# Kernel optimization log

Hardware: AMD Instinct MI355X
Metric: run time of the kernel (lower is better)

Reference implementation:

```python
import jax, jax.numpy as jnp
import numpy as np

THRESHOLD = 0.05


def ternary_project(w, threshold=THRESHOLD, use_ste=True):
    # scale: mean |w| over all axes except the last (per-output-column scale)
    reduce_axes = tuple(range(w.ndim - 1))
    scale = jnp.mean(jnp.abs(w), axis=reduce_axes, keepdims=True)
    ternary = jnp.where(jnp.abs(w) < threshold, 0.0, jnp.sign(w)) * scale
    if use_ste:
        return w + jax.lax.stop_gradient(ternary - w)
    return ternary


def setup_inputs() -> dict:
    key = jax.random.key(0)
    kx, kw = jax.random.split(key)
    B, S, D, O = 8, 2048, 4096, 4096
    x = jax.random.normal(kx, (B, S, D), dtype=jnp.float32)
    w = jax.random.normal(kw, (D, O), dtype=jnp.float32) * 0.02  # small init like VarianceScaling
    b = jnp.zeros((O,), dtype=jnp.float32)
    return {"x": x, "w": w, "b": b}


def reference(x, w, b):
    y = x @ ternary_project(w, threshold=THRESHOLD, use_ste=True)
    return y + b
```

## Files before the change

### kernel.cpp

```cpp
#include <hip/hip_runtime.h>
#include <stdint.h>

typedef int i32x4 __attribute__((ext_vector_type(4)));

#define D_DIM 4096
#define O_DIM 4096
#define M_DIM 16384
#define THRESH 0.05f


__device__ __forceinline__ void gld16(const void* g, void* l) {
  __builtin_amdgcn_global_load_lds(
      (const __attribute__((address_space(1))) uint32_t*)(uintptr_t)g,
      (__attribute__((address_space(3))) uint32_t*)(uint32_t)(uintptr_t)l,
      16, 0, 0);
}

__device__ __forceinline__ int tern_i8(float v) {
  return (__builtin_fabsf(v) < THRESH) ? 0 : (v > 0.f ? 1 : -1);
}


__global__ void k_scale_part(const float* __restrict__ w, float* __restrict__ part) {
  const int cg = blockIdx.x & 63;
  const int dz = blockIdx.x >> 6;
  const int tx = threadIdx.x & 63;
  const int ty = threadIdx.x >> 6;
  const int o = cg * 64 + tx;
  float s = 0.f;
  const float* p = w + (size_t)(dz * 512 + ty) * O_DIM + o;
  for (int i = 0; i < 128; ++i) {
    s += __builtin_fabsf(*p);
    p += 4 * O_DIM;
  }
  __shared__ float red[4][64];
  red[ty][tx] = s;
  __syncthreads();
  if (ty == 0) part[dz * O_DIM + o] = (red[0][tx] + red[1][tx]) + (red[2][tx] + red[3][tx]);
}

__global__ void k_scale_fin(const float* __restrict__ part, float* __restrict__ scale) {
  const int o = blockIdx.x * 256 + threadIdx.x;
  float s = 0.f;
#pragma unroll
  for (int z = 0; z < 8; ++z) s += part[z * O_DIM + o];
  scale[o] = s * (1.0f / 4096.0f);
}

__global__ void k_tern_q(const float* __restrict__ w, char* __restrict__ btq) {
  __shared__ char tile[64][68];
  const int ot = blockIdx.x & 63;
  const int dt = blockIdx.x >> 6;
  const int o0 = ot * 64, d0 = dt * 64;
  const int tx = threadIdx.x & 15, ty = threadIdx.x >> 4;
#pragma unroll
  for (int j = 0; j < 4; ++j) {
    const int r = ty + 16 * j;
    const float4 v = *(const float4*)&w[(size_t)(d0 + r) * O_DIM + o0 + tx * 4];
    uint32_t u = (uint32_t)(tern_i8(v.x) & 0xFF) |
                 ((uint32_t)(tern_i8(v.y) & 0xFF) << 8) |
                 ((uint32_t)(tern_i8(v.z) & 0xFF) << 16) |
                 ((uint32_t)(tern_i8(v.w) & 0xFF) << 24);
    *(uint32_t*)&tile[r][tx * 4] = u;
  }
  __syncthreads();
#pragma unroll
  for (int j = 0; j < 4; ++j) {
    const int orow = ty + 16 * j;
    uint32_t u = (uint32_t)((uint8_t)tile[tx * 4 + 0][orow]) |
                 ((uint32_t)((uint8_t)tile[tx * 4 + 1][orow]) << 8) |
                 ((uint32_t)((uint8_t)tile[tx * 4 + 2][orow]) << 16) |
                 ((uint32_t)((uint8_t)tile[tx * 4 + 3][orow]) << 24);
    *(uint32_t*)&btq[(size_t)(o0 + orow) * D_DIM + d0 + tx * 4] = u;
  }
}

__global__ void k_quant(const float* __restrict__ x, char* __restrict__ xq,
                        float* __restrict__ sx) {
  const int row = blockIdx.x;
  const int t = threadIdx.x;
  const float* xr = x + (size_t)row * D_DIM + t * 16;
  float4 v[4];
#pragma unroll
  for (int i = 0; i < 4; ++i) v[i] = *(const float4*)(xr + i * 4);
  float m = 0.f;
#pragma unroll
  for (int i = 0; i < 4; ++i) {
    m = fmaxf(m, fmaxf(fmaxf(__builtin_fabsf(v[i].x), __builtin_fabsf(v[i].y)),
                       fmaxf(__builtin_fabsf(v[i].z), __builtin_fabsf(v[i].w))));
  }
#pragma unroll
  for (int off = 32; off >= 1; off >>= 1) m = fmaxf(m, __shfl_xor(m, off, 64));
  __shared__ float wm[4];
  if ((t & 63) == 0) wm[t >> 6] = m;
  __syncthreads();
  const float rm = fmaxf(fmaxf(wm[0], wm[1]), fmaxf(wm[2], wm[3]));
  const float inv = (rm > 0.f) ? 127.0f / rm : 0.0f;
  int4 o;
  int* op = (int*)&o;
#pragma unroll
  for (int i = 0; i < 4; ++i) {
    const float* f = (const float*)&v[i];
    uint32_t u = 0;
#pragma unroll
    for (int j = 0; j < 4; ++j) {
      float q = __builtin_rintf(f[j] * inv);
      q = fmaxf(-127.f, fminf(127.f, q));
      u |= ((uint32_t)((int)q & 0xFF)) << (8 * j);
    }
    op[i] = (int)u;
  }
  *(int4*)(xq + (size_t)row * D_DIM + t * 16) = o;
  if (t == 0) sx[row] = (rm > 0.f) ? rm * (1.0f / 127.0f) : 0.0f;
}


#define BAR() __builtin_amdgcn_s_barrier()
#define SB0() __builtin_amdgcn_sched_barrier(0)
#define LGKM0()                                         \
  do {                                                  \
    asm volatile("s_waitcnt lgkmcnt(0)" ::: "memory");  \
    __builtin_amdgcn_sched_barrier(0);                  \
  } while (0)
#define VMW(n) asm volatile("s_waitcnt vmcnt(" #n ")" ::: "memory")

#define STAGE_A(d, h, kv)                                                    \
  do {                                                                       \
    gld16(pA##h##_0 + (size_t)(kv) * 128,                                    \
          smem + (d)*32768 + (h)*16384 + t * 16);                            \
    gld16(pA##h##_1 + (size_t)(kv) * 128,                                    \
          smem + (d)*32768 + (h)*16384 + 8192 + t * 16);                     \
  } while (0)
#define STAGE_B(d, h, kv)                                                    \
  do {                                                                       \
    gld16(pB##h##_0 + (size_t)(kv) * 128,                                    \
          smem + 65536 + (d)*32768 + (h)*16384 + t * 16);                    \
    gld16(pB##h##_1 + (size_t)(kv) * 128,                                    \
          smem + 65536 + (d)*32768 + (h)*16384 + 8192 + t * 16);             \
  } while (0)

#define READ_A(d, mh)                                                   \
  do {                                                                  \
    const char* ab_ = smem + (d)*32768 + wr * 16384 + (mh)*8192;        \
    _Pragma("unroll") for (int m4 = 0; m4 < 4; ++m4) {                  \
      aq[mh][0][m4] = *(const i32x4*)(ab_ + m4 * 2048 + aLane);         \
      aq[mh][1][m4] = *(const i32x4*)(ab_ + m4 * 2048 + (aLane ^ 64));  \
    }                                                                   \
  } while (0)

#define READ_B(db, pp)                                                       \
  do {                                                                       \
    const char* bb_ = smem + 65536 + (db)*32768 + hb * 16384 + hw8192;       \
    _Pragma("unroll") for (int nh = 0; nh < 2; ++nh)                         \
    _Pragma("unroll") for (int n2 = 0; n2 < 2; ++n2) {                       \
      bq[pp][nh][0][n2] =                                                    \
          *(const i32x4*)(bb_ + nh * 4096 + n2 * 2048 + aLane);              \
      bq[pp][nh][1][n2] =                                                    \
          *(const i32x4*)(bb_ + nh * 4096 + n2 * 2048 + (aLane ^ 64));       \
    }                                                                        \
  } while (0)

#define MQ(mh, nh, pp)                                                        \
  do {                                                                        \
    __builtin_amdgcn_s_setprio(1);                                            \
    _Pragma("unroll") for (int kk = 0; kk < 2; ++kk)                          \
    _Pragma("unroll") for (int m4 = 0; m4 < 4; ++m4)                          \
    _Pragma("unroll") for (int n2 = 0; n2 < 2; ++n2)                          \
        acc[(mh)*4 + m4][(nh)*2 + n2] =                                       \
            __builtin_amdgcn_mfma_i32_16x16x64_i8(                            \
                aq[mh][kk][m4], bq[pp][nh][kk][n2],                           \
                acc[(mh)*4 + m4][(nh)*2 + n2], 0, 0, 0);                      \
    __builtin_amdgcn_s_setprio(0);                                            \
  } while (0)

#define TILE(d, pp, kv)                                                  \
  do {                                                                   \
    READ_A(d, 0); STAGE_B(d, 0, kv);                                     \
    BAR(); LGKM0(); MQ(0, 0, pp); BAR();                                 \
    READ_A(d, 1); STAGE_B(d, 1, kv);                                     \
    BAR(); LGKM0(); MQ(0, 1, pp); BAR();                                 \
    STAGE_A(d, 0, kv);                                                   \
    BAR(); __builtin_amdgcn_sched_barrier(0); MQ(1, 0, pp); VMW(10);     \
    BAR();                                                               \
    READ_B((d) ^ 1, (pp) ^ 1); STAGE_A(d, 1, kv);                        \
    BAR(); __builtin_amdgcn_sched_barrier(0); MQ(1, 1, pp); VMW(8);      \
    BAR();                                                               \
  } while (0)

__global__ __launch_bounds__(512, 2) void k_gemm8(
    const char* __restrict__ A,
    const char* __restrict__ B,
    const float* __restrict__ sx, const float* __restrict__ scale,
    const float* __restrict__ bias, float* __restrict__ C) {
  __shared__ __align__(16) char smem[131072];

  const int bid = blockIdx.x;
  const int wg = (bid & 7) * 128 + (bid >> 3);
  const int mb = wg >> 4, nb = wg & 15;
  const int mBase = mb * 256, nBase = nb * 256;

  const int t = threadIdx.x;
  const int lane = t & 63, wid = t >> 6;
  const int wr = wid >> 2, wc = wid & 3;
  const int hb = wc >> 1;
  const int hw8192 = (wc & 1) * 8192;
  const int r16 = lane & 15, kq = lane >> 4;
  const int aLane = r16 * 128 + ((kq ^ (lane & 7)) << 4);

  const int q1 = 512 + t;
  const int sr0 = t >> 3, sg0 = (t & 7) ^ (sr0 & 7);
  const int sr1 = q1 >> 3, sg1 = (q1 & 7) ^ (sr1 & 7);

  const char* pA0_0 = A + (size_t)(mBase + sr0) * D_DIM + sg0 * 16;
  const char* pA0_1 = A + (size_t)(mBase + sr1) * D_DIM + sg1 * 16;
  const char* pA1_0 = A + (size_t)(mBase + 128 + sr0) * D_DIM + sg0 * 16;
  const char* pA1_1 = A + (size_t)(mBase + 128 + sr1) * D_DIM + sg1 * 16;
  const char* pB0_0 = B + (size_t)(nBase + sr0) * D_DIM + sg0 * 16;
  const char* pB0_1 = B + (size_t)(nBase + sr1) * D_DIM + sg1 * 16;
  const char* pB1_0 = B + (size_t)(nBase + 128 + sr0) * D_DIM + sg0 * 16;
  const char* pB1_1 = B + (size_t)(nBase + 128 + sr1) * D_DIM + sg1 * 16;

  i32x4 acc[8][4] = {};
  i32x4 aq[2][2][4];
  i32x4 bq[2][2][2][2];

  STAGE_B(0, 0, 0); STAGE_B(0, 1, 0); STAGE_A(0, 0, 0); STAGE_A(0, 1, 0);
  STAGE_B(1, 0, 1); STAGE_B(1, 1, 1); STAGE_A(1, 0, 1); STAGE_A(1, 1, 1);
  VMW(8);
  BAR();
  RB_PROLOGUE:;
  READ_B(0, 0);
  LGKM0();
  BAR();

  for (int T = 0; T < 32; T += 2) {
    TILE(0, 0, (T + 2) & 31);
    TILE(1, 1, (T + 3) & 31);
  }
  VMW(0);

  float sxr[8][4];
#pragma unroll
  for (int mi = 0; mi < 8; ++mi) {
    const int gr0 = mBase + wr * 128 + mi * 16 + kq * 4;
#pragma unroll
    for (int r = 0; r < 4; ++r) sxr[mi][r] = sx[gr0 + r];
  }
#pragma unroll
  for (int ni = 0; ni < 4; ++ni) {
    const int gc = nBase + wc * 64 + ni * 16 + r16;
    const float sw = scale[gc];
    const float bb = bias[gc];
#pragma unroll
    for (int mi = 0; mi < 8; ++mi) {
      const int gr0 = mBase + wr * 128 + mi * 16 + kq * 4;
#pragma unroll
      for (int r = 0; r < 4; ++r) {
        C[(size_t)(gr0 + r) * O_DIM + gc] =
            (float)acc[mi][ni][r] * (sxr[mi][r] * sw) + bb;
      }
    }
  }
}


extern "C" void kernel_launch(void* const* d_in, const int* in_sizes, int n_in,
                              void* d_out, int out_size, void* d_ws, size_t ws_size,
                              hipStream_t stream) {
  const float* x = (const float*)d_in[0];
  const float* w = (const float*)d_in[1];
  const float* bias = (const float*)d_in[2];
  float* out = (float*)d_out;

  const size_t XQ_OFF = 0;
  const size_t BT_OFF = (size_t)M_DIM * D_DIM;
  const size_t SX_OFF = BT_OFF + (size_t)O_DIM * D_DIM;
  const size_t PART_OFF = SX_OFF + (size_t)M_DIM * 4;
  const size_t SCALE_OFF = PART_OFF + 8 * O_DIM * 4;
  const size_t NEED = SCALE_OFF + O_DIM * 4;
  if (ws_size < NEED) return;

  char* ws = (char*)d_ws;
  char* xq = ws + XQ_OFF;
  char* btq = ws + BT_OFF;
  float* sx = (float*)(ws + SX_OFF);
  float* part = (float*)(ws + PART_OFF);
  float* scale = (float*)(ws + SCALE_OFF);

  k_scale_part<<<512, 256, 0, stream>>>(w, part);
  k_scale_fin<<<16, 256, 0, stream>>>(part, scale);
  k_tern_q<<<64 * 64, 256, 0, stream>>>(w, btq);
  k_quant<<<M_DIM, 256, 0, stream>>>(x, xq, sx);
  k_gemm8<<<1024, 512, 0, stream>>>(xq, btq, sx, scale, bias, out);
}
```

Before: 373.5 us.

## Fuse weight scale reduction into ternary quantize and restructure GEMM LDS schedule

The separate k_scale_part pass over w is removed. Per-column |w| partial sums are now computed inside k_tern_q from the already-loaded tile and written to a 64-way partial buffer, which k_scale_fin then reduces. Separately, the GEMM inner tile schedule is reorganized: both A halves are read before the first MFMA group, waits become partial lgkmcnt counts, and fewer barriers are used, so LDS reads overlap more with MFMA work. This trades one fewer read of w for a larger partial buffer and a riskier wait/barrier ordering.

```diff
diff --git a/kernel.cpp b/kernel.cpp
--- a/kernel.cpp
+++ b/kernel.cpp
@@ -21,48 +21,32 @@
 }
 
 
-__global__ void k_scale_part(const float* __restrict__ w, float* __restrict__ part) {
-  const int cg = blockIdx.x & 63;
-  const int dz = blockIdx.x >> 6;
-  const int tx = threadIdx.x & 63;
-  const int ty = threadIdx.x >> 6;
-  const int o = cg * 64 + tx;
-  float s = 0.f;
-  const float* p = w + (size_t)(dz * 512 + ty) * O_DIM + o;
-  for (int i = 0; i < 128; ++i) {
-    s += __builtin_fabsf(*p);
-    p += 4 * O_DIM;
-  }
-  __shared__ float red[4][64];
-  red[ty][tx] = s;
-  __syncthreads();
-  if (ty == 0) part[dz * O_DIM + o] = (red[0][tx] + red[1][tx]) + (red[2][tx] + red[3][tx]);
-}
-
-__global__ void k_scale_fin(const float* __restrict__ part, float* __restrict__ scale) {
-  const int o = blockIdx.x * 256 + threadIdx.x;
-  float s = 0.f;
-#pragma unroll
-  for (int z = 0; z < 8; ++z) s += part[z * O_DIM + o];
-  scale[o] = s * (1.0f / 4096.0f);
-}
-
-__global__ void k_tern_q(const float* __restrict__ w, char* __restrict__ btq) {
+__global__ void k_tern_q(const float* __restrict__ w, char* __restrict__ btq,
+                         float* __restrict__ part) {
   __shared__ char tile[64][68];
+  __shared__ float sred[16][68];
   const int ot = blockIdx.x & 63;
   const int dt = blockIdx.x >> 6;
   const int o0 = ot * 64, d0 = dt * 64;
-  const int tx = threadIdx.x & 15, ty = threadIdx.x >> 4;
+  const int t = threadIdx.x;
+  const int tx = t & 15, ty = t >> 4;
+  float s0 = 0.f, s1 = 0.f, s2 = 0.f, s3 = 0.f;
 #pragma unroll
   for (int j = 0; j < 4; ++j) {
     const int r = ty + 16 * j;
     const float4 v = *(const float4*)&w[(size_t)(d0 + r) * O_DIM + o0 + tx * 4];
+    s0 += __builtin_fabsf(v.x); s1 += __builtin_fabsf(v.y);
+    s2 += __builtin_fabsf(v.z); s3 += __builtin_fabsf(v.w);
     uint32_t u = (uint32_t)(tern_i8(v.x) & 0xFF) |
                  ((uint32_t)(tern_i8(v.y) & 0xFF) << 8) |
                  ((uint32_t)(tern_i8(v.z) & 0xFF) << 16) |
                  ((uint32_t)(tern_i8(v.w) & 0xFF) << 24);
     *(uint32_t*)&tile[r][tx * 4] = u;
   }
+  sred[ty][tx * 4 + 0] = s0;
+  sred[ty][tx * 4 + 1] = s1;
+  sred[ty][tx * 4 + 2] = s2;
+  sred[ty][tx * 4 + 3] = s3;
   __syncthreads();
 #pragma unroll
   for (int j = 0; j < 4; ++j) {
@@ -73,6 +57,20 @@
                  ((uint32_t)((uint8_t)tile[tx * 4 + 3][orow]) << 24);
     *(uint32_t*)&btq[(size_t)(o0 + orow) * D_DIM + d0 + tx * 4] = u;
   }
+  if (t < 64) {
+    float s = 0.f;
+#pragma unroll
+    for (int i = 0; i < 16; ++i) s += sred[i][t];
+    part[(size_t)dt * O_DIM + o0 + t] = s;
+  }
+}
+
+__global__ void k_scale_fin(const float* __restrict__ part, float* __restrict__ scale) {
+  const int o = blockIdx.x * 256 + threadIdx.x;
+  float s = 0.f;
+#pragma unroll
+  for (int z = 0; z < 64; ++z) s += part[(size_t)z * O_DIM + o];
+  scale[o] = s * (1.0f / 4096.0f);
 }
 
 __global__ void k_quant(const float* __restrict__ x, char* __restrict__ xq,
@@ -117,11 +115,7 @@
 
 #define BAR() __builtin_amdgcn_s_barrier()
 #define SB0() __builtin_amdgcn_sched_barrier(0)
-#define LGKM0()                                         \
-  do {                                                  \
-    asm volatile("s_waitcnt lgkmcnt(0)" ::: "memory");  \
-    __builtin_amdgcn_sched_barrier(0);                  \
-  } while (0)
+#define LGKM(n) asm volatile("s_waitcnt lgkmcnt(" #n ")" ::: "memory")
 #define VMW(n) asm volatile("s_waitcnt vmcnt(" #n ")" ::: "memory")
 
 #define STAGE_A(d, h, kv)                                                    \
@@ -175,15 +169,16 @@
 
 #define TILE(d, pp, kv)                                                  \
   do {                                                                   \
-    READ_A(d, 0); STAGE_B(d, 0, kv);                                     \
-    BAR(); LGKM0(); MQ(0, 0, pp); BAR();                                 \
-    READ_A(d, 1); STAGE_B(d, 1, kv);                                     \
-    BAR(); LGKM0(); MQ(0, 1, pp); BAR();                                 \
-    STAGE_A(d, 0, kv);                                                   \
-    BAR(); __builtin_amdgcn_sched_barrier(0); MQ(1, 0, pp); VMW(10);     \
+    READ_A(d, 0); READ_A(d, 1); STAGE_B(d, 0, kv); STAGE_B(d, 1, kv);    \
+    BAR(); LGKM(8); SB0();                                               \
+    MQ(0, 0, pp); MQ(0, 1, pp);                                          \
     BAR();                                                               \
-    READ_B((d) ^ 1, (pp) ^ 1); STAGE_A(d, 1, kv);                        \
-    BAR(); __builtin_amdgcn_sched_barrier(0); MQ(1, 1, pp); VMW(8);      \
+    STAGE_A(d, 0, kv); STAGE_A(d, 1, kv);                                \
+    LGKM(0); SB0();                                                      \
+    MQ(1, 0, pp);                                                        \
+    VMW(8); BAR();                                                       \
+    READ_B((d) ^ 1, (pp) ^ 1); SB0();                                    \
+    MQ(1, 1, pp);                                                        \
     BAR();                                                               \
   } while (0)
 
@@ -228,9 +223,8 @@
   STAGE_B(1, 0, 1); STAGE_B(1, 1, 1); STAGE_A(1, 0, 1); STAGE_A(1, 1, 1);
   VMW(8);
   BAR();
-  RB_PROLOGUE:;
   READ_B(0, 0);
-  LGKM0();
+  LGKM(0); SB0();
   BAR();
 
   for (int T = 0; T < 32; T += 2) {
@@ -276,7 +270,7 @@
   const size_t BT_OFF = (size_t)M_DIM * D_DIM;
   const size_t SX_OFF = BT_OFF + (size_t)O_DIM * D_DIM;
   const size_t PART_OFF = SX_OFF + (size_t)M_DIM * 4;
-  const size_t SCALE_OFF = PART_OFF + 8 * O_DIM * 4;
+  const size_t SCALE_OFF = PART_OFF + (size_t)64 * O_DIM * 4;
   const size_t NEED = SCALE_OFF + O_DIM * 4;
   if (ws_size < NEED) return;
 
@@ -287,9 +281,8 @@
   float* part = (float*)(ws + PART_OFF);
   float* scale = (float*)(ws + SCALE_OFF);
 
-  k_scale_part<<<512, 256, 0, stream>>>(w, part);
+  k_tern_q<<<64 * 64, 256, 0, stream>>>(w, btq, part);
   k_scale_fin<<<16, 256, 0, stream>>>(part, scale);
-  k_tern_q<<<64 * 64, 256, 0, stream>>>(w, btq);
   k_quant<<<M_DIM, 256, 0, stream>>>(x, xq, sx);
   k_gemm8<<<1024, 512, 0, stream>>>(xq, btq, sx, scale, bias, out);
 }
```

Result: slower. 381.4 us (+2.1%).

## Shrink int8 GEMM tile to 128x128 with 256-thread blocks and simpler pipeline

Applied to the files above, without the earlier changes.

Replaces the 256x256 tile, 512-thread GEMM with a 128x128 tile, 4-wave block using 64 KiB LDS. Each wave now computes a 64x64 output sub-tile, and the staging and compute schedule per K step is simplified. The block remap changes so that each XCD handles a contiguous band of N columns. Smaller tiles cut per-block LDS and registers, which may allow more resident blocks, but they halve data reuse and double global and LDS traffic per MFMA.

```diff
diff --git a/kernel.cpp b/kernel.cpp
--- a/kernel.cpp
+++ b/kernel.cpp
@@ -117,132 +117,121 @@
 
 #define BAR() __builtin_amdgcn_s_barrier()
 #define SB0() __builtin_amdgcn_sched_barrier(0)
-#define LGKM0()                                         \
-  do {                                                  \
-    asm volatile("s_waitcnt lgkmcnt(0)" ::: "memory");  \
-    __builtin_amdgcn_sched_barrier(0);                  \
-  } while (0)
+#define LGKM(n) asm volatile("s_waitcnt lgkmcnt(" #n ")" ::: "memory")
 #define VMW(n) asm volatile("s_waitcnt vmcnt(" #n ")" ::: "memory")
 
-#define STAGE_A(d, h, kv)                                                    \
-  do {                                                                       \
-    gld16(pA##h##_0 + (size_t)(kv) * 128,                                    \
-          smem + (d)*32768 + (h)*16384 + t * 16);                            \
-    gld16(pA##h##_1 + (size_t)(kv) * 128,                                    \
-          smem + (d)*32768 + (h)*16384 + 8192 + t * 16);                     \
-  } while (0)
-#define STAGE_B(d, h, kv)                                                    \
-  do {                                                                       \
-    gld16(pB##h##_0 + (size_t)(kv) * 128,                                    \
-          smem + 65536 + (d)*32768 + (h)*16384 + t * 16);                    \
-    gld16(pB##h##_1 + (size_t)(kv) * 128,                                    \
-          smem + 65536 + (d)*32768 + (h)*16384 + 8192 + t * 16);             \
-  } while (0)
-
-#define READ_A(d, mh)                                                   \
-  do {                                                                  \
-    const char* ab_ = smem + (d)*32768 + wr * 16384 + (mh)*8192;        \
-    _Pragma("unroll") for (int m4 = 0; m4 < 4; ++m4) {                  \
-      aq[mh][0][m4] = *(const i32x4*)(ab_ + m4 * 2048 + aLane);         \
-      aq[mh][1][m4] = *(const i32x4*)(ab_ + m4 * 2048 + (aLane ^ 64));  \
-    }                                                                   \
-  } while (0)
-
-#define READ_B(db, pp)                                                       \
-  do {                                                                       \
-    const char* bb_ = smem + 65536 + (db)*32768 + hb * 16384 + hw8192;       \
-    _Pragma("unroll") for (int nh = 0; nh < 2; ++nh)                         \
-    _Pragma("unroll") for (int n2 = 0; n2 < 2; ++n2) {                       \
-      bq[pp][nh][0][n2] =                                                    \
-          *(const i32x4*)(bb_ + nh * 4096 + n2 * 2048 + aLane);              \
-      bq[pp][nh][1][n2] =                                                    \
-          *(const i32x4*)(bb_ + nh * 4096 + n2 * 2048 + (aLane ^ 64));       \
-    }                                                                        \
-  } while (0)
-
-#define MQ(mh, nh, pp)                                                        \
+#define STAGE_A(d, kv)                                              \
+  do {                                                              \
+    gld16(pA0 + (size_t)(kv) * 128, smem + (d)*16384 + t * 16);     \
+    gld16(pA1 + (size_t)(kv) * 128, smem + (d)*16384 + 4096 + t * 16); \
+    gld16(pA2 + (size_t)(kv) * 128, smem + (d)*16384 + 8192 + t * 16); \
+    gld16(pA3 + (size_t)(kv) * 128, smem + (d)*16384 + 12288 + t * 16); \
+  } while (0)
+#define STAGE_B(d, kv)                                              \
+  do {                                                              \
+    gld16(pB0 + (size_t)(kv) * 128, smem + 32768 + (d)*16384 + t * 16); \
+    gld16(pB1 + (size_t)(kv) * 128, smem + 32768 + (d)*16384 + 4096 + t * 16); \
+    gld16(pB2 + (size_t)(kv) * 128, smem + 32768 + (d)*16384 + 8192 + t * 16); \
+    gld16(pB3 + (size_t)(kv) * 128, smem + 32768 + (d)*16384 + 12288 + t * 16); \
+  } while (0)
+
+#define RA(d)                                                          \
+  do {                                                                 \
+    const char* ab_ = smem + (d)*16384 + (wr * 64 + r16) * 128;        \
+    _Pragma("unroll") for (int m4 = 0; m4 < 4; ++m4) {                 \
+      aq[0][m4] = *(const i32x4*)(ab_ + m4 * 2048 + slot0);            \
+      aq[1][m4] = *(const i32x4*)(ab_ + m4 * 2048 + (slot0 ^ 64));     \
+    }                                                                  \
+  } while (0)
+#define RB(db)                                                         \
+  do {                                                                 \
+    const char* bb_ = smem + 32768 + (db)*16384 + (wc * 64 + r16) * 128; \
+    _Pragma("unroll") for (int n4 = 0; n4 < 4; ++n4) {                 \
+      bq[0][n4] = *(const i32x4*)(bb_ + n4 * 2048 + slot0);            \
+      bq[1][n4] = *(const i32x4*)(bb_ + n4 * 2048 + (slot0 ^ 64));     \
+    }                                                                  \
+  } while (0)
+
+#define MQ(kk)                                                                \
   do {                                                                        \
     __builtin_amdgcn_s_setprio(1);                                            \
-    _Pragma("unroll") for (int kk = 0; kk < 2; ++kk)                          \
     _Pragma("unroll") for (int m4 = 0; m4 < 4; ++m4)                          \
-    _Pragma("unroll") for (int n2 = 0; n2 < 2; ++n2)                          \
-        acc[(mh)*4 + m4][(nh)*2 + n2] =                                       \
-            __builtin_amdgcn_mfma_i32_16x16x64_i8(                            \
-                aq[mh][kk][m4], bq[pp][nh][kk][n2],                           \
-                acc[(mh)*4 + m4][(nh)*2 + n2], 0, 0, 0);                      \
+    _Pragma("unroll") for (int n4 = 0; n4 < 4; ++n4)                          \
+        acc[m4][n4] = __builtin_amdgcn_mfma_i32_16x16x64_i8(                  \
+            aq[kk][m4], bq[kk][n4], acc[m4][n4], 0, 0, 0);                    \
     __builtin_amdgcn_s_setprio(0);                                            \
   } while (0)
 
-#define TILE(d, pp, kv)                                                  \
+#define TILE(d, kv)                                                      \
   do {                                                                   \
-    READ_A(d, 0); STAGE_B(d, 0, kv);                                     \
-    BAR(); LGKM0(); MQ(0, 0, pp); BAR();                                 \
-    READ_A(d, 1); STAGE_B(d, 1, kv);                                     \
-    BAR(); LGKM0(); MQ(0, 1, pp); BAR();                                 \
-    STAGE_A(d, 0, kv);                                                   \
-    BAR(); __builtin_amdgcn_sched_barrier(0); MQ(1, 0, pp); VMW(10);     \
+    RA(d);                                                               \
+    STAGE_B(d, kv);                                                      \
+    BAR(); LGKM(4); SB0();                                               \
+    MQ(0);                                                               \
     BAR();                                                               \
-    READ_B((d) ^ 1, (pp) ^ 1); STAGE_A(d, 1, kv);                        \
-    BAR(); __builtin_amdgcn_sched_barrier(0); MQ(1, 1, pp); VMW(8);      \
+    STAGE_A(d, kv);                                                      \
+    LGKM(0); SB0();                                                      \
+    MQ(1);                                                               \
+    VMW(8); BAR();                                                       \
+    RB((d) ^ 1); SB0();                                                  \
     BAR();                                                               \
   } while (0)
 
-__global__ __launch_bounds__(512, 2) void k_gemm8(
+__global__ __launch_bounds__(256, 2) void k_gemm8(
     const char* __restrict__ A,
     const char* __restrict__ B,
     const float* __restrict__ sx, const float* __restrict__ scale,
     const float* __restrict__ bias, float* __restrict__ C) {
-  __shared__ __align__(16) char smem[131072];
+  __shared__ __align__(16) char smem[65536];
 
   const int bid = blockIdx.x;
-  const int wg = (bid & 7) * 128 + (bid >> 3);
-  const int mb = wg >> 4, nb = wg & 15;
-  const int mBase = mb * 256, nBase = nb * 256;
+  const int xcd = bid & 7, s = bid >> 3;
+  const int nb = xcd * 4 + (s >> 7);
+  const int mb = s & 127;
+  const int mBase = mb * 128, nBase = nb * 128;
 
   const int t = threadIdx.x;
   const int lane = t & 63, wid = t >> 6;
-  const int wr = wid >> 2, wc = wid & 3;
-  const int hb = wc >> 1;
-  const int hw8192 = (wc & 1) * 8192;
+  const int wr = wid >> 1, wc = wid & 1;
   const int r16 = lane & 15, kq = lane >> 4;
-  const int aLane = r16 * 128 + ((kq ^ (lane & 7)) << 4);
-
-  const int q1 = 512 + t;
+  const int slot0 = (kq ^ (r16 & 7)) << 4;
+
   const int sr0 = t >> 3, sg0 = (t & 7) ^ (sr0 & 7);
+  const int q1 = 256 + t, q2 = 512 + t, q3 = 768 + t;
   const int sr1 = q1 >> 3, sg1 = (q1 & 7) ^ (sr1 & 7);
-
-  const char* pA0_0 = A + (size_t)(mBase + sr0) * D_DIM + sg0 * 16;
-  const char* pA0_1 = A + (size_t)(mBase + sr1) * D_DIM + sg1 * 16;
-  const char* pA1_0 = A + (size_t)(mBase + 128 + sr0) * D_DIM + sg0 * 16;
-  const char* pA1_1 = A + (size_t)(mBase + 128 + sr1) * D_DIM + sg1 * 16;
-  const char* pB0_0 = B + (size_t)(nBase + sr0) * D_DIM + sg0 * 16;
-  const char* pB0_1 = B + (size_t)(nBase + sr1) * D_DIM + sg1 * 16;
-  const char* pB1_0 = B + (size_t)(nBase + 128 + sr0) * D_DIM + sg0 * 16;
-  const char* pB1_1 = B + (size_t)(nBase + 128 + sr1) * D_DIM + sg1 * 16;
-
-  i32x4 acc[8][4] = {};
-  i32x4 aq[2][2][4];
-  i32x4 bq[2][2][2][2];
-
-  STAGE_B(0, 0, 0); STAGE_B(0, 1, 0); STAGE_A(0, 0, 0); STAGE_A(0, 1, 0);
-  STAGE_B(1, 0, 1); STAGE_B(1, 1, 1); STAGE_A(1, 0, 1); STAGE_A(1, 1, 1);
+  const int sr2 = q2 >> 3, sg2 = (q2 & 7) ^ (sr2 & 7);
+  const int sr3 = q3 >> 3, sg3 = (q3 & 7) ^ (sr3 & 7);
+
+  const char* pA0 = A + (size_t)(mBase + sr0) * D_DIM + sg0 * 16;
+  const char* pA1 = A + (size_t)(mBase + sr1) * D_DIM + sg1 * 16;
+  const char* pA2 = A + (size_t)(mBase + sr2) * D_DIM + sg2 * 16;
+  const char* pA3 = A + (size_t)(mBase + sr3) * D_DIM + sg3 * 16;
+  const char* pB0 = B + (size_t)(nBase + sr0) * D_DIM + sg0 * 16;
+  const char* pB1 = B + (size_t)(nBase + sr1) * D_DIM + sg1 * 16;
+  const char* pB2 = B + (size_t)(nBase + sr2) * D_DIM + sg2 * 16;
+  const char* pB3 = B + (size_t)(nBase + sr3) * D_DIM + sg3 * 16;
+
+  i32x4 acc[4][4] = {};
+  i32x4 aq[2][4];
+  i32x4 bq[2][4];
+
+  STAGE_A(0, 0); STAGE_B(0, 0);
+  STAGE_A(1, 1); STAGE_B(1, 1);
   VMW(8);
   BAR();
-  RB_PROLOGUE:;
-  READ_B(0, 0);
-  LGKM0();
+  RB(0);
   BAR();
 
   for (int T = 0; T < 32; T += 2) {
-    TILE(0, 0, (T + 2) & 31);
-    TILE(1, 1, (T + 3) & 31);
+    TILE(0, (T + 2) & 31);
+    TILE(1, (T + 3) & 31);
   }
   VMW(0);
 
-  float sxr[8][4];
-#pragma unroll
-  for (int mi = 0; mi < 8; ++mi) {
-    const int gr0 = mBase + wr * 128 + mi * 16 + kq * 4;
+  float sxr[4][4];
+#pragma unroll
+  for (int mi = 0; mi < 4; ++mi) {
+    const int gr0 = mBase + wr * 64 + mi * 16 + kq * 4;
 #pragma unroll
     for (int r = 0; r < 4; ++r) sxr[mi][r] = sx[gr0 + r];
   }
@@ -252,8 +241,8 @@
     const float sw = scale[gc];
     const float bb = bias[gc];
 #pragma unroll
-    for (int mi = 0; mi < 8; ++mi) {
-      const int gr0 = mBase + wr * 128 + mi * 16 + kq * 4;
+    for (int mi = 0; mi < 4; ++mi) {
+      const int gr0 = mBase + wr * 64 + mi * 16 + kq * 4;
 #pragma unroll
       for (int r = 0; r < 4; ++r) {
         C[(size_t)(gr0 + r) * O_DIM + gc] =
@@ -291,5 +280,5 @@
   k_scale_fin<<<16, 256, 0, stream>>>(part, scale);
   k_tern_q<<<64 * 64, 256, 0, stream>>>(w, btq);
   k_quant<<<M_DIM, 256, 0, stream>>>(x, xq, sx);
-  k_gemm8<<<1024, 512, 0, stream>>>(xq, btq, sx, scale, bias, out);
-}
+  k_gemm8<<<4096, 256, 0, stream>>>(xq, btq, sx, scale, bias, out);
+}
```

After: 479.6 us. 1.28x slower.
